# Kernel optimization log

Hardware: AMD Instinct MI355X
Metric: run time of the kernel (lower is better)

The kernel has to match this reference:

```python
import jax, jax.numpy as jnp
import numpy as np

B, S, EMBED = 8, 2048, 768
NQ = 8            # n_qubits == ffn_dim
N_QLAYERS = 2
DIM = 2 ** NQ     # state-vector size


def _apply_single(state, mat, wire):
    """Apply a 2x2 gate on `wire`. state: (T, 2**NQ) complex. mat: (2,2) or (T,2,2)."""
    a, b = 2 ** wire, 2 ** (NQ - wire - 1)
    s = state.reshape(-1, a, 2, b)
    if mat.ndim == 2:
        out = jnp.einsum('ij,tajb->taib', mat, s)
    else:
        out = jnp.einsum('tij,tajb->taib', mat, s)
    return out.reshape(state.shape)


def _apply_cnot(state, ctrl, tgt):
    s = state.reshape((-1,) + (2,) * NQ)
    s = jnp.moveaxis(s, (ctrl + 1, tgt + 1), (-2, -1))
    # where control bit == 1, flip target bit
    s = jnp.stack([s[..., 0, :], s[..., 1, ::-1]], axis=-2)
    s = jnp.moveaxis(s, (-2, -1), (ctrl + 1, tgt + 1))
    return s.reshape(state.shape)


def _rx_mats(angles):
    """Batched RX gates. angles: (T,) -> (T,2,2) complex."""
    c = jnp.cos(angles / 2).astype(jnp.complex64)
    s = (-1j) * jnp.sin(angles / 2).astype(jnp.complex64)
    return jnp.stack([jnp.stack([c, s], -1), jnp.stack([s, c], -1)], -2)


def _ry_mat(angle):
    c = jnp.cos(angle / 2).astype(jnp.complex64)
    s = jnp.sin(angle / 2).astype(jnp.complex64)
    return jnp.stack([jnp.stack([c, -s], -1), jnp.stack([s, c], -1)], -2)


def _circuit(angles, theta):
    """angles: (T, NQ) RX encode angles; theta: (NQ,) trainable RY angles.
    Returns PauliZ expectation per wire: (T, NQ)."""
    T = angles.shape[0]
    state = jnp.zeros((T, DIM), dtype=jnp.complex64).at[:, 0].set(1.0)
    # RX encoder, one gate per wire, angle per token
    for w in range(NQ):
        state = _apply_single(state, _rx_mats(angles[:, w]), w)
    # trainable RY per wire
    for w in range(NQ):
        state = _apply_single(state, _ry_mat(theta[w]), w)
    # entangling CNOT ring, (n_qlayers - 1) times
    for _ in range(N_QLAYERS - 1):
        for w in range(NQ - 1):
            state = _apply_cnot(state, w, w + 1)
        state = _apply_cnot(state, NQ - 1, 0)
    probs = state.real ** 2 + state.imag ** 2  # (T, DIM)
    exps = []
    for w in range(NQ):
        a, b = 2 ** w, 2 ** (NQ - w - 1)
        p = probs.reshape(-1, a, 2, b)
        exps.append(p[:, :, 0, :].sum((1, 2)) - p[:, :, 1, :].sum((1, 2)))
    return jnp.stack(exps, axis=-1)  # (T, NQ)


def setup_inputs() -> dict:
    key = jax.random.key(0)
    ks = jax.random.split(key, 6)
    return {
        'x': jax.random.normal(ks[0], (B, S, EMBED), dtype=jnp.float32),
        'W1': jax.random.normal(ks[1], (NQ, EMBED), dtype=jnp.float32) * (1.0 / np.sqrt(EMBED)),
        'b1': jax.random.normal(ks[2], (NQ,), dtype=jnp.float32) * 0.02,
        'theta': jax.random.normal(ks[3], (NQ,), dtype=jnp.float32),
        'W2': jax.random.normal(ks[4], (EMBED, NQ), dtype=jnp.float32) * (1.0 / np.sqrt(NQ)),
        'b2': jax.random.normal(ks[5], (EMBED,), dtype=jnp.float32) * 0.02,
    }


def reference(x, W1, b1, theta, W2, b2):
    # linear1: embed -> n_qubits (RX encode angles)
    q_in = jnp.einsum('bse,qe->bsq', x, W1) + b1          # (B, S, NQ)
    z = _circuit(q_in.reshape(-1, NQ), theta)             # (B*S, NQ)
    z = z.reshape(B, S, NQ)
    # dropout is identity in eval; noise_scale = 0
    out = jnp.einsum('bsq,eq->bse', z, W2) + b2           # (B, S, EMBED)
    return jax.nn.relu(out)
```

## Files before the change

### kernel.cpp

```cpp
#include <hip/hip_runtime.h>
#include <math.h>


constexpr int EMBED = 768;
constexpr int NQ    = 8;
constexpr int BLOCK = 256;
constexpr int WAVES = 4;
constexpr int TPT   = 2;
constexpr int TPB   = WAVES * TPT;

typedef float vfloat4 __attribute__((ext_vector_type(4)));

__global__ __launch_bounds__(BLOCK, 6) void ffq_kernel(
    const float* __restrict__ x,  const float* __restrict__ W1,
    const float* __restrict__ b1, const float* __restrict__ theta,
    const float* __restrict__ W2, const float* __restrict__ b2,
    float* __restrict__ out, int ntok)
{
    __shared__ float w2t[NQ][EMBED];
    __shared__ float zbuf[WAVES][TPT][NQ];

    const int tid  = threadIdx.x;
    const int wave = tid >> 6;
    const int lane = tid & 63;

    const int t0 = (blockIdx.x * WAVES + wave) * TPT;
    int tk[TPT];
    #pragma unroll
    for (int it = 0; it < TPT; ++it) {
        int t = t0 + it; tk[it] = (t < ntok) ? t : (ntok - 1);
    }

    const float4* x4 = (const float4*)x;
    float4 xv[TPT][3];
    #pragma unroll
    for (int it = 0; it < TPT; ++it)
        #pragma unroll
        for (int k = 0; k < 3; ++k)
            xv[it][k] = x4[(size_t)tk[it] * (EMBED / 4) + lane + 64 * k];

    {
        const float4* W24 = (const float4*)W2;
        for (int i = tid; i < EMBED * NQ / 4; i += BLOCK) {
            const float4 v = W24[i];
            const int f = 4 * i;
            w2t[(f + 0) & 7][(f + 0) >> 3] = v.x;
            w2t[(f + 1) & 7][(f + 1) >> 3] = v.y;
            w2t[(f + 2) & 7][(f + 2) >> 3] = v.z;
            w2t[(f + 3) & 7][(f + 3) >> 3] = v.w;
        }
    }

    const int q_own = lane & 7;
    const float costh = __cosf(theta[q_own]);
    const float b1q   = b1[q_own];

    __syncthreads();

    const float4* W14 = (const float4*)W1;
    float acc[TPT][NQ];
    #pragma unroll
    for (int it = 0; it < TPT; ++it)
        #pragma unroll
        for (int q = 0; q < NQ; ++q) acc[it][q] = 0.f;

    #pragma unroll
    for (int k = 0; k < 3; ++k) {
        const int idx = lane + 64 * k;
        #pragma unroll
        for (int q = 0; q < NQ; ++q) {
            const float4 w = W14[q * (EMBED / 4) + idx];
            #pragma unroll
            for (int it = 0; it < TPT; ++it) {
                acc[it][q] = fmaf(xv[it][k].x, w.x, fmaf(xv[it][k].y, w.y,
                             fmaf(xv[it][k].z, w.z, fmaf(xv[it][k].w, w.w, acc[it][q]))));
            }
        }
    }

    const bool c0 = lane & 1, c1 = lane & 2, c2 = lane & 4;
    float S[TPT];
    #pragma unroll
    for (int it = 0; it < TPT; ++it) {
        float k0 = c0 ? acc[it][1] : acc[it][0], g0 = c0 ? acc[it][0] : acc[it][1];
        float k1 = c0 ? acc[it][3] : acc[it][2], g1 = c0 ? acc[it][2] : acc[it][3];
        float k2 = c0 ? acc[it][5] : acc[it][4], g2 = c0 ? acc[it][4] : acc[it][5];
        float k3 = c0 ? acc[it][7] : acc[it][6], g3 = c0 ? acc[it][6] : acc[it][7];
        float v0 = k0 + __shfl_xor(g0, 1, 64);
        float v1 = k1 + __shfl_xor(g1, 1, 64);
        float v2 = k2 + __shfl_xor(g2, 1, 64);
        float v3 = k3 + __shfl_xor(g3, 1, 64);
        float ka = c1 ? v1 : v0, ga = c1 ? v0 : v1;
        float kb = c1 ? v3 : v2, gb = c1 ? v2 : v3;
        float u0 = ka + __shfl_xor(ga, 2, 64);
        float u1 = kb + __shfl_xor(gb, 2, 64);
        float kc = c2 ? u1 : u0, gc = c2 ? u0 : u1;
        float s  = kc + __shfl_xor(gc, 4, 64);
        s += __shfl_xor(s, 8, 64);
        s += __shfl_xor(s, 16, 64);
        s += __shfl_xor(s, 32, 64);
        S[it] = s;
    }

    const int osel = (lane >> 3) & (TPT - 1);
    const float Ssel = osel ? S[1] : S[0];
    const float zval = costh * __cosf(Ssel + b1q);
    zbuf[wave][osel][q_own] = zval;

    float ex[TPT][NQ];
    #pragma unroll
    for (int it = 0; it < TPT; ++it) {
        const float4 za = ((const float4*)zbuf[wave][it])[0];
        const float4 zb = ((const float4*)zbuf[wave][it])[1];
        const float zq[NQ] = { za.x, za.y, za.z, za.w, zb.x, zb.y, zb.z, zb.w };
        float p = zq[0];
        #pragma unroll
        for (int q = 1; q < NQ; ++q) { p *= zq[q]; ex[it][q] = p; }
        float sfx = zq[1];
        #pragma unroll
        for (int q = 2; q < NQ; ++q) sfx *= zq[q];
        ex[it][0] = sfx;
    }

    const float4* b24 = (const float4*)b2;
    #pragma unroll
    for (int k = 0; k < 3; ++k) {
        const int idx = lane + 64 * k;
        const float4 bb = b24[idx];
        float4 r[TPT];
        #pragma unroll
        for (int it = 0; it < TPT; ++it) r[it] = bb;
        #pragma unroll
        for (int q = 0; q < NQ; ++q) {
            const float4 w = ((const float4*)&w2t[q][0])[idx];
            #pragma unroll
            for (int it = 0; it < TPT; ++it) {
                r[it].x = fmaf(ex[it][q], w.x, r[it].x);
                r[it].y = fmaf(ex[it][q], w.y, r[it].y);
                r[it].z = fmaf(ex[it][q], w.z, r[it].z);
                r[it].w = fmaf(ex[it][q], w.w, r[it].w);
            }
        }
        #pragma unroll
        for (int it = 0; it < TPT; ++it) {
            vfloat4 o = { fmaxf(r[it].x, 0.f), fmaxf(r[it].y, 0.f),
                          fmaxf(r[it].z, 0.f), fmaxf(r[it].w, 0.f) };
            __builtin_nontemporal_store(o, (vfloat4*)(out + (size_t)tk[it] * EMBED) + idx);
        }
    }
}

extern "C" void kernel_launch(void* const* d_in, const int* in_sizes, int n_in,
                              void* d_out, int out_size, void* d_ws, size_t ws_size,
                              hipStream_t stream) {
    const float* x     = (const float*)d_in[0];
    const float* W1    = (const float*)d_in[1];
    const float* b1    = (const float*)d_in[2];
    const float* theta = (const float*)d_in[3];
    const float* W2    = (const float*)d_in[4];
    const float* b2    = (const float*)d_in[5];
    float* out = (float*)d_out;

    const int ntok = in_sizes[0] / EMBED;
    const int grid = (ntok + TPB - 1) / TPB;
    hipLaunchKernelGGL(ffq_kernel, dim3(grid), dim3(BLOCK), 0, stream,
                       x, W1, b1, theta, W2, b2, out, ntok);
}
```

Before: 25.95 us.

## Split fused kernel into encode and output kernels with workspace handoff

Result: slower. 29.21 us (+12.6%).

```diff
diff --git a/kernel.cpp b/kernel.cpp
--- a/kernel.cpp
+++ b/kernel.cpp
@@ -11,81 +11,53 @@
 
 typedef float vfloat4 __attribute__((ext_vector_type(4)));
 
-__global__ __launch_bounds__(BLOCK, 6) void ffq_kernel(
+__global__ __launch_bounds__(BLOCK, 8) void ffq_zkern(
     const float* __restrict__ x,  const float* __restrict__ W1,
     const float* __restrict__ b1, const float* __restrict__ theta,
-    const float* __restrict__ W2, const float* __restrict__ b2,
-    float* __restrict__ out, int ntok)
+    const float* __restrict__ W2,
+    float* __restrict__ zws, float* __restrict__ w2t, int ntok)
 {
-    __shared__ float w2t[NQ][EMBED];
-    __shared__ float zbuf[WAVES][TPT][NQ];
-
     const int tid  = threadIdx.x;
     const int wave = tid >> 6;
     const int lane = tid & 63;
-
-    const int t0 = (blockIdx.x * WAVES + wave) * TPT;
-    int tk[TPT];
-    #pragma unroll
-    for (int it = 0; it < TPT; ++it) {
-        int t = t0 + it; tk[it] = (t < ntok) ? t : (ntok - 1);
-    }
+    const int t0   = (blockIdx.x * WAVES + wave) * TPT;
+    const int ta   = min(t0, ntok - 1);
+    const int tb   = min(t0 + 1, ntok - 1);
 
     const float4* x4 = (const float4*)x;
-    float4 xv[TPT][3];
-    #pragma unroll
-    for (int it = 0; it < TPT; ++it)
-        #pragma unroll
-        for (int k = 0; k < 3; ++k)
-            xv[it][k] = x4[(size_t)tk[it] * (EMBED / 4) + lane + 64 * k];
-
-    {
-        const float4* W24 = (const float4*)W2;
-        for (int i = tid; i < EMBED * NQ / 4; i += BLOCK) {
-            const float4 v = W24[i];
-            const int f = 4 * i;
-            w2t[(f + 0) & 7][(f + 0) >> 3] = v.x;
-            w2t[(f + 1) & 7][(f + 1) >> 3] = v.y;
-            w2t[(f + 2) & 7][(f + 2) >> 3] = v.z;
-            w2t[(f + 3) & 7][(f + 3) >> 3] = v.w;
-        }
-    }
-
-    const int q_own = lane & 7;
-    const float costh = __cosf(theta[q_own]);
-    const float b1q   = b1[q_own];
-
-    __syncthreads();
+    const float4 xa0 = x4[(size_t)ta * (EMBED / 4) + lane];
+    const float4 xa1 = x4[(size_t)ta * (EMBED / 4) + lane + 64];
+    const float4 xa2 = x4[(size_t)ta * (EMBED / 4) + lane + 128];
+    const float4 xb0 = x4[(size_t)tb * (EMBED / 4) + lane];
+    const float4 xb1 = x4[(size_t)tb * (EMBED / 4) + lane + 64];
+    const float4 xb2 = x4[(size_t)tb * (EMBED / 4) + lane + 128];
 
     const float4* W14 = (const float4*)W1;
-    float acc[TPT][NQ];
+    float acc0[NQ], acc1[NQ];
     #pragma unroll
-    for (int it = 0; it < TPT; ++it)
-        #pragma unroll
-        for (int q = 0; q < NQ; ++q) acc[it][q] = 0.f;
-
+    for (int q = 0; q < NQ; ++q) { acc0[q] = 0.f; acc1[q] = 0.f; }
     #pragma unroll
-    for (int k = 0; k < 3; ++k) {
-        const int idx = lane + 64 * k;
-        #pragma unroll
-        for (int q = 0; q < NQ; ++q) {
-            const float4 w = W14[q * (EMBED / 4) + idx];
-            #pragma unroll
-            for (int it = 0; it < TPT; ++it) {
-                acc[it][q] = fmaf(xv[it][k].x, w.x, fmaf(xv[it][k].y, w.y,
-                             fmaf(xv[it][k].z, w.z, fmaf(xv[it][k].w, w.w, acc[it][q]))));
-            }
-        }
+    for (int q = 0; q < NQ; ++q) {
+        const float4 w0 = W14[q * (EMBED / 4) + lane];
+        const float4 w1 = W14[q * (EMBED / 4) + lane + 64];
+        const float4 w2 = W14[q * (EMBED / 4) + lane + 128];
+        float s0 = 0.f, s1 = 0.f;
+        s0 = fmaf(xa0.x, w0.x, fmaf(xa0.y, w0.y, fmaf(xa0.z, w0.z, fmaf(xa0.w, w0.w, s0))));
+        s0 = fmaf(xa1.x, w1.x, fmaf(xa1.y, w1.y, fmaf(xa1.z, w1.z, fmaf(xa1.w, w1.w, s0))));
+        s0 = fmaf(xa2.x, w2.x, fmaf(xa2.y, w2.y, fmaf(xa2.z, w2.z, fmaf(xa2.w, w2.w, s0))));
+        s1 = fmaf(xb0.x, w0.x, fmaf(xb0.y, w0.y, fmaf(xb0.z, w0.z, fmaf(xb0.w, w0.w, s1))));
+        s1 = fmaf(xb1.x, w1.x, fmaf(xb1.y, w1.y, fmaf(xb1.z, w1.z, fmaf(xb1.w, w1.w, s1))));
+        s1 = fmaf(xb2.x, w2.x, fmaf(xb2.y, w2.y, fmaf(xb2.z, w2.z, fmaf(xb2.w, w2.w, s1))));
+        acc0[q] = s0; acc1[q] = s1;
     }
 
     const bool c0 = lane & 1, c1 = lane & 2, c2 = lane & 4;
-    float S[TPT];
-    #pragma unroll
-    for (int it = 0; it < TPT; ++it) {
-        float k0 = c0 ? acc[it][1] : acc[it][0], g0 = c0 ? acc[it][0] : acc[it][1];
-        float k1 = c0 ? acc[it][3] : acc[it][2], g1 = c0 ? acc[it][2] : acc[it][3];
-        float k2 = c0 ? acc[it][5] : acc[it][4], g2 = c0 ? acc[it][4] : acc[it][5];
-        float k3 = c0 ? acc[it][7] : acc[it][6], g3 = c0 ? acc[it][6] : acc[it][7];
+    float S0, S1;
+    {
+        float k0 = c0 ? acc0[1] : acc0[0], g0 = c0 ? acc0[0] : acc0[1];
+        float k1 = c0 ? acc0[3] : acc0[2], g1 = c0 ? acc0[2] : acc0[3];
+        float k2 = c0 ? acc0[5] : acc0[4], g2 = c0 ? acc0[4] : acc0[5];
+        float k3 = c0 ? acc0[7] : acc0[6], g3 = c0 ? acc0[6] : acc0[7];
         float v0 = k0 + __shfl_xor(g0, 1, 64);
         float v1 = k1 + __shfl_xor(g1, 1, 64);
         float v2 = k2 + __shfl_xor(g2, 1, 64);
@@ -99,54 +71,100 @@
         s += __shfl_xor(s, 8, 64);
         s += __shfl_xor(s, 16, 64);
         s += __shfl_xor(s, 32, 64);
-        S[it] = s;
+        S0 = s;
+    }
+    {
+        float k0 = c0 ? acc1[1] : acc1[0], g0 = c0 ? acc1[0] : acc1[1];
+        float k1 = c0 ? acc1[3] : acc1[2], g1 = c0 ? acc1[2] : acc1[3];
+        float k2 = c0 ? acc1[5] : acc1[4], g2 = c0 ? acc1[4] : acc1[5];
+        float k3 = c0 ? acc1[7] : acc1[6], g3 = c0 ? acc1[6] : acc1[7];
+        float v0 = k0 + __shfl_xor(g0, 1, 64);
+        float v1 = k1 + __shfl_xor(g1, 1, 64);
+        float v2 = k2 + __shfl_xor(g2, 1, 64);
+        float v3 = k3 + __shfl_xor(g3, 1, 64);
+        float ka = c1 ? v1 : v0, ga = c1 ? v0 : v1;
+        float kb = c1 ? v3 : v2, gb = c1 ? v2 : v3;
+        float u0 = ka + __shfl_xor(ga, 2, 64);
+        float u1 = kb + __shfl_xor(gb, 2, 64);
+        float kc = c2 ? u1 : u0, gc = c2 ? u0 : u1;
+        float s  = kc + __shfl_xor(gc, 4, 64);
+        s += __shfl_xor(s, 8, 64);
+        s += __shfl_xor(s, 16, 64);
+        s += __shfl_xor(s, 32, 64);
+        S1 = s;
     }
 
-    const int osel = (lane >> 3) & (TPT - 1);
-    const float Ssel = osel ? S[1] : S[0];
-    const float zval = costh * __cosf(Ssel + b1q);
-    zbuf[wave][osel][q_own] = zval;
+    const int q_own = lane & 7;
+    const int osel  = (lane >> 3) & 1;
+    const float zval = __cosf(theta[q_own]) * __cosf((osel ? S1 : S0) + b1[q_own]);
+    if (lane < 16) zws[(size_t)t0 * NQ + lane] = zval;
 
-    float ex[TPT][NQ];
-    #pragma unroll
-    for (int it = 0; it < TPT; ++it) {
-        const float4 za = ((const float4*)zbuf[wave][it])[0];
-        const float4 zb = ((const float4*)zbuf[wave][it])[1];
-        const float zq[NQ] = { za.x, za.y, za.z, za.w, zb.x, zb.y, zb.z, zb.w };
+    if (blockIdx.x == 0) {
+        for (int o = tid; o < NQ * EMBED; o += BLOCK)
+            w2t[o] = W2[(o % EMBED) * NQ + (o / EMBED)];
+    }
+}
+
+__global__ __launch_bounds__(BLOCK, 8) void ffq_okern(
+    const float* __restrict__ zws, const float* __restrict__ w2t,
+    const float* __restrict__ b2,  float* __restrict__ out, int ntok)
+{
+    const int tid  = threadIdx.x;
+    const int wave = tid >> 6;
+    const int lane = tid & 63;
+    const int t0   = (blockIdx.x * WAVES + wave) * TPT;
+    const int ta   = min(t0, ntok - 1);
+    const int tb   = min(t0 + 1, ntok - 1);
+
+    const float4* z4 = (const float4*)(zws + (size_t)t0 * NQ);
+    const float4 za0 = z4[0], za1 = z4[1];
+    const float4 zb0 = z4[2], zb1 = z4[3];
+
+    float ex0[NQ], ex1[NQ];
+    {
+        const float zq[NQ] = { za0.x, za0.y, za0.z, za0.w, za1.x, za1.y, za1.z, za1.w };
         float p = zq[0];
         #pragma unroll
-        for (int q = 1; q < NQ; ++q) { p *= zq[q]; ex[it][q] = p; }
+        for (int q = 1; q < NQ; ++q) { p *= zq[q]; ex0[q] = p; }
         float sfx = zq[1];
         #pragma unroll
         for (int q = 2; q < NQ; ++q) sfx *= zq[q];
-        ex[it][0] = sfx;
+        ex0[0] = sfx;
+    }
+    {
+        const float zq[NQ] = { zb0.x, zb0.y, zb0.z, zb0.w, zb1.x, zb1.y, zb1.z, zb1.w };
+        float p = zq[0];
+        #pragma unroll
+        for (int q = 1; q < NQ; ++q) { p *= zq[q]; ex1[q] = p; }
+        float sfx = zq[1];
+        #pragma unroll
+        for (int q = 2; q < NQ; ++q) sfx *= zq[q];
+        ex1[0] = sfx;
     }
 
-    const float4* b24 = (const float4*)b2;
+    const float4* W2T4 = (const float4*)w2t;
+    const float4* b24  = (const float4*)b2;
     #pragma unroll
     for (int k = 0; k < 3; ++k) {
         const int idx = lane + 64 * k;
         const float4 bb = b24[idx];
-        float4 r[TPT];
-        #pragma unroll
-        for (int it = 0; it < TPT; ++it) r[it] = bb;
+        float4 r0 = bb, r1 = bb;
         #pragma unroll
         for (int q = 0; q < NQ; ++q) {
-            const float4 w = ((const float4*)&w2t[q][0])[idx];
-            #pragma unroll
-            for (int it = 0; it < TPT; ++it) {
-                r[it].x = fmaf(ex[it][q], w.x, r[it].x);
-                r[it].y = fmaf(ex[it][q], w.y, r[it].y);
-                r[it].z = fmaf(ex[it][q], w.z, r[it].z);
-                r[it].w = fmaf(ex[it][q], w.w, r[it].w);
-            }
+            const float4 w = W2T4[q * (EMBED / 4) + idx];
+            r0.x = fmaf(ex0[q], w.x, r0.x);
+            r0.y = fmaf(ex0[q], w.y, r0.y);
+            r0.z = fmaf(ex0[q], w.z, r0.z);
+            r0.w = fmaf(ex0[q], w.w, r0.w);
+            r1.x = fmaf(ex1[q], w.x, r1.x);
+            r1.y = fmaf(ex1[q], w.y, r1.y);
+            r1.z = fmaf(ex1[q], w.z, r1.z);
+            r1.w = fmaf(ex1[q], w.w, r1.w);
         }
-        #pragma unroll
-        for (int it = 0; it < TPT; ++it) {
-            vfloat4 o = { fmaxf(r[it].x, 0.f), fmaxf(r[it].y, 0.f),
-                          fmaxf(r[it].z, 0.f), fmaxf(r[it].w, 0.f) };
-            __builtin_nontemporal_store(o, (vfloat4*)(out + (size_t)tk[it] * EMBED) + idx);
-        }
+        vfloat4 o0 = { fmaxf(r0.x, 0.f), fmaxf(r0.y, 0.f), fmaxf(r0.z, 0.f), fmaxf(r0.w, 0.f) };
+        vfloat4 o1 = { fmaxf(r1.x, 0.f), fmaxf(r1.y, 0.f), fmaxf(r1.z, 0.f), fmaxf(r1.w, 0.f) };
+        __builtin_nontemporal_store(o0, (vfloat4*)(out + (size_t)ta * EMBED) + idx);
+        __builtin_nontemporal_store(o1, (vfloat4*)(out + (size_t)tb * EMBED) + idx);
     }
 }
 
@@ -162,7 +180,12 @@
     float* out = (float*)d_out;
 
     const int ntok = in_sizes[0] / EMBED;
+    float* zws = (float*)d_ws;
+    float* w2t = zws + (size_t)ntok * NQ;
+
     const int grid = (ntok + TPB - 1) / TPB;
-    hipLaunchKernelGGL(ffq_kernel, dim3(grid), dim3(BLOCK), 0, stream,
-                       x, W1, b1, theta, W2, b2, out, ntok);
+    hipLaunchKernelGGL(ffq_zkern, dim3(grid), dim3(BLOCK), 0, stream,
+                       x, W1, b1, theta, W2, zws, w2t, ntok);
+    hipLaunchKernelGGL(ffq_okern, dim3(grid), dim3(BLOCK), 0, stream,
+                       zws, w2t, b2, out, ntok);
 }
```
